# Kernel tuning notes

Hardware: AMD Instinct MI355X
Metric: run time of the kernel (lower is better)

Reference implementation:

```python
import jax, jax.numpy as jnp
import numpy as np
from jax import lax

DIM = 512          # model dim
L = 32             # img_size
N = L * L          # tokens
H = 4              # heads
C = DIM // 4       # channels per Res2Net scale
D = C // H         # per-head dim = 32 (== dim_head)
B = 8
SCALE = 32 ** -0.5  # dim_head ** -0.5
EPS = 1e-5


def setup_inputs() -> dict:
    key = jax.random.key(0)
    ks = jax.random.split(key, 13)
    nrm = lambda k, s, std: jax.random.normal(k, s, jnp.float32) * std
    uni = lambda k, s: jax.random.uniform(k, s, jnp.float32, 0.5, 1.5)
    return {
        "x": nrm(ks[0], (B, N, DIM), 1.0),
        "w_in": nrm(ks[1], (DIM, DIM), DIM ** -0.5),
        "bn1_g": uni(ks[2], (DIM,)),
        "bn1_b": nrm(ks[3], (DIM,), 0.1),
        "bn1_m": nrm(ks[4], (DIM,), 0.1),
        "bn1_v": uni(ks[5], (DIM,)),
        "w_dw": nrm(ks[6], (C, 1, 3, 3), 1.0 / 3.0),
        "w_pw": nrm(ks[7], (C, C), C ** -0.5),
        "bn2_g": uni(ks[8], (C,)),
        "bn2_b": nrm(ks[9], (C,), 0.1),
        "bn2_m": nrm(ks[10], (C,), 0.1),
        "bn2_v": uni(ks[11], (C,)),
        "w_out": nrm(ks[12], (DIM, DIM), DIM ** -0.5),
    }


def _bn(x, g, b, m, v):
    # eval-mode BatchNorm2d over NCHW
    inv = g / jnp.sqrt(v + EPS)
    return x * inv[None, :, None, None] + (b - m * inv)[None, :, None, None]


def _forward(x, w_in, bn1_g, bn1_b, bn1_m, bn1_v,
             w_dw, w_pw, bn2_g, bn2_b, bn2_m, bn2_v, w_out):
    b = x.shape[0]
    # 'b (l w) n -> b n l w'
    xi = x.transpose(0, 2, 1).reshape(b, DIM, L, L)
    # Res2Net: inconv (1x1 conv + BN)
    ident = jnp.einsum('oc,bchw->bohw', w_in, xi)
    ident = _bn(ident, bn1_g, bn1_b, bn1_m, bn1_v)
    xs = jnp.split(ident, 4, axis=1)

    def x3conv(t):
        t = lax.conv_general_dilated(
            t, w_dw, window_strides=(1, 1), padding='SAME',
            feature_group_count=C,
            dimension_numbers=('NCHW', 'OIHW', 'NCHW'))
        t = jnp.einsum('oc,bchw->bohw', w_pw, t)
        return _bn(t, bn2_g, bn2_b, bn2_m, bn2_v)

    ys = [xs[0]]
    ys.append(x3conv(xs[1]))
    ys.append(x3conv(xs[2] + ys[1]))
    ys.append(x3conv(xs[3] + ys[2]))
    y = jnp.stack(ys, axis=1)  # [b, 4, C, L, L]

    # 'b (h d) l w -> b h (l w) d' per scale; batch the 4 scales together
    qkv = y.reshape(b, 4, H, D, N).transpose(0, 1, 2, 4, 3)  # [b,4,h,n,d]
    att = jnp.einsum('bshid,bshjd->bshij', qkv, qkv) * SCALE   # [b,4,h,n,n]
    att = jax.nn.softmax(att, axis=-1)
    o = jnp.einsum('bshij,bshjd->bshid', att, qkv)             # [b,4,h,n,d]
    # cat over scales of 'b h n d -> b n (h d)' => [b, n, (s h d)] = [b, n, DIM]
    o = o.transpose(0, 3, 1, 2, 4).reshape(b, N, DIM)
    return o @ w_out.T  # Linear(dim, dim, bias=False); dropout is identity (eval)


def reference(x, w_in, bn1_g, bn1_b, bn1_m, bn1_v,
              w_dw, w_pw, bn2_g, bn2_b, bn2_m, bn2_v, w_out):
    return _forward(x, w_in, bn1_g, bn1_b, bn1_m, bn1_v,
                    w_dw, w_pw, bn2_g, bn2_b, bn2_m, bn2_v, w_out)
```

## Files before the change

### kernel.cpp

```cpp
#include <hip/hip_runtime.h>
#include <hip/hip_bf16.h>


#define DIMM 512
#define NTOK 1024
#define CC   128
#define DD   32
#define BB   8
#define EPSB 1e-5f
#define SCALE_ATT 0.17677669529663687f
#define K2EXP (SCALE_ATT * 1.4426950408889634f)
#define TJ 128

typedef __attribute__((ext_vector_type(8))) short short8;
typedef __attribute__((ext_vector_type(4))) float f32x4;

__device__ __forceinline__ unsigned short f2bf(float f) {
    unsigned int x = __float_as_uint(f);
    unsigned int r = x + 0x7fffu + ((x >> 16) & 1u);
    return (unsigned short)(r >> 16);
}
__device__ __forceinline__ unsigned int f2bf2(float lo, float hi) {
    return (unsigned int)f2bf(lo) | ((unsigned int)f2bf(hi) << 16);
}

__global__ __launch_bounds__(256) void k_mm_in(
    const float* __restrict__ w_in,
    const float* __restrict__ x,
    const float* __restrict__ g1, const float* __restrict__ b1,
    const float* __restrict__ m1, const float* __restrict__ v1,
    float* __restrict__ Y)
{
    __shared__ __align__(16) unsigned short As[128][72];
    __shared__ __align__(16) unsigned short Bs[128][72];
    const int r0 = blockIdx.x * 128;
    const int o0 = blockIdx.y * 128;
    const int b  = r0 >> 10, nloc0 = r0 & 1023;
    const int t = threadIdx.x, wid = t >> 6, lane = t & 63;
    const int l16 = lane & 15, quad = lane >> 4;
    const int wm = (wid >> 1) * 64, wn = (wid & 1) * 64;

    f32x4 acc[4][4];
#pragma unroll
    for (int i = 0; i < 4; i++)
#pragma unroll
        for (int j = 0; j < 4; j++) acc[i][j] = (f32x4){0.f, 0.f, 0.f, 0.f};

    for (int k0 = 0; k0 < DIMM; k0 += 64) {
        __syncthreads();
#pragma unroll
        for (int it = 0; it < 8; it++) {
            int flat = it * 256 + t;
            int row = flat >> 4, c4 = flat & 15;
            float4 w4 = *(const float4*)&w_in[(size_t)(o0 + row) * DIMM + k0 + c4 * 4];
            *(uint2*)&As[row][c4 * 4] = make_uint2(f2bf2(w4.x, w4.y), f2bf2(w4.z, w4.w));
            float4 x4 = *(const float4*)&x[(size_t)(r0 + row) * DIMM + k0 + c4 * 4];
            *(uint2*)&Bs[row][c4 * 4] = make_uint2(f2bf2(x4.x, x4.y), f2bf2(x4.z, x4.w));
        }
        __syncthreads();
#pragma unroll
        for (int kk = 0; kk < 2; kk++) {
            short8 af[4], bf_[4];
#pragma unroll
            for (int i = 0; i < 4; i++) af[i]  = *(const short8*)&As[wm + i * 16 + l16][kk * 32 + quad * 8];
#pragma unroll
            for (int j = 0; j < 4; j++) bf_[j] = *(const short8*)&Bs[wn + j * 16 + l16][kk * 32 + quad * 8];
#pragma unroll
            for (int i = 0; i < 4; i++)
#pragma unroll
                for (int j = 0; j < 4; j++)
                    acc[i][j] = __builtin_amdgcn_mfma_f32_16x16x32_bf16(af[i], bf_[j], acc[i][j], 0, 0, 0);
        }
    }
#pragma unroll
    for (int i = 0; i < 4; i++)
#pragma unroll
        for (int r = 0; r < 4; r++) {
            int o = o0 + wm + i * 16 + quad * 4 + r;
            float inv  = g1[o] / sqrtf(v1[o] + EPSB);
            float beta = b1[o] - m1[o] * inv;
#pragma unroll
            for (int j = 0; j < 4; j++) {
                int n = nloc0 + wn + j * 16 + l16;
                Y[((size_t)b * DIMM + o) * NTOK + n] = acc[i][j][r] * inv + beta;
            }
        }
}

__global__ __launch_bounds__(256) void k_dwconv(
    const float* __restrict__ Y, const float* __restrict__ w_dw,
    float* __restrict__ tmp, int s)
{
    __shared__ float img[34][34];
    const int c = blockIdx.x;
    const int b = blockIdx.y;
    const int t = threadIdx.x;
    for (int i = t; i < 34 * 34; i += 256) (&img[0][0])[i] = 0.f;
    __syncthreads();
    const float* src0 = Y + ((size_t)b * DIMM + s * CC + c) * NTOK;
    const float* src1 = (s >= 2) ? (Y + ((size_t)b * DIMM + (s - 1) * CC + c) * NTOK) : nullptr;
    for (int p = t; p < NTOK; p += 256) {
        float v = src0[p];
        if (src1) v += src1[p];
        img[(p >> 5) + 1][(p & 31) + 1] = v;
    }
    __syncthreads();
    float w[9];
#pragma unroll
    for (int i = 0; i < 9; i++) w[i] = w_dw[c * 9 + i];
    for (int p = t; p < NTOK; p += 256) {
        int yy = p >> 5, xx = p & 31;
        float s0 = 0.f;
#pragma unroll
        for (int ky = 0; ky < 3; ky++)
#pragma unroll
            for (int kx = 0; kx < 3; kx++)
                s0 += img[yy + ky][xx + kx] * w[ky * 3 + kx];
        tmp[((size_t)b * CC + c) * NTOK + p] = s0;
    }
}

__global__ __launch_bounds__(256) void k_mm_pw(
    const float* __restrict__ tmp, const float* __restrict__ w_pw,
    const float* __restrict__ g2, const float* __restrict__ b2,
    const float* __restrict__ m2, const float* __restrict__ v2,
    float* __restrict__ Y, int s)
{
    __shared__ __align__(16) unsigned short As[128][72];
    __shared__ __align__(16) unsigned short Bs[64][72];
    const int n0 = blockIdx.x * 64;
    const int b  = blockIdx.y;
    const int t = threadIdx.x, wid = t >> 6, lane = t & 63;
    const int l16 = lane & 15, quad = lane >> 4;
    const int wm = (wid >> 1) * 64, wn = (wid & 1) * 32;

    f32x4 acc[4][2];
#pragma unroll
    for (int i = 0; i < 4; i++) { acc[i][0] = (f32x4){0.f,0.f,0.f,0.f}; acc[i][1] = (f32x4){0.f,0.f,0.f,0.f}; }

    for (int k0 = 0; k0 < CC; k0 += 64) {
        __syncthreads();
#pragma unroll
        for (int it = 0; it < 8; it++) {
            int flat = it * 256 + t;
            int row = flat >> 4, c4 = flat & 15;
            float4 w4 = *(const float4*)&w_pw[(size_t)row * CC + k0 + c4 * 4];
            *(uint2*)&As[row][c4 * 4] = make_uint2(f2bf2(w4.x, w4.y), f2bf2(w4.z, w4.w));
        }
#pragma unroll
        for (int it = 0; it < 4; it++) {
            int flat = it * 256 + t;
            int c = flat >> 4, n4 = (flat & 15) * 4;
            float4 v = *(const float4*)&tmp[((size_t)b * CC + k0 + c) * NTOK + n0 + n4];
            Bs[n4 + 0][c] = f2bf(v.x);
            Bs[n4 + 1][c] = f2bf(v.y);
            Bs[n4 + 2][c] = f2bf(v.z);
            Bs[n4 + 3][c] = f2bf(v.w);
        }
        __syncthreads();
#pragma unroll
        for (int kk = 0; kk < 2; kk++) {
            short8 af[4], bf_[2];
#pragma unroll
            for (int i = 0; i < 4; i++) af[i]  = *(const short8*)&As[wm + i * 16 + l16][kk * 32 + quad * 8];
#pragma unroll
            for (int j = 0; j < 2; j++) bf_[j] = *(const short8*)&Bs[wn + j * 16 + l16][kk * 32 + quad * 8];
#pragma unroll
            for (int i = 0; i < 4; i++)
#pragma unroll
                for (int j = 0; j < 2; j++)
                    acc[i][j] = __builtin_amdgcn_mfma_f32_16x16x32_bf16(af[i], bf_[j], acc[i][j], 0, 0, 0);
        }
    }
#pragma unroll
    for (int i = 0; i < 4; i++)
#pragma unroll
        for (int r = 0; r < 4; r++) {
            int o = wm + i * 16 + quad * 4 + r;
            float inv  = g2[o] / sqrtf(v2[o] + EPSB);
            float beta = b2[o] - m2[o] * inv;
#pragma unroll
            for (int j = 0; j < 2; j++) {
                int n = n0 + wn + j * 16 + l16;
                Y[((size_t)b * DIMM + s * CC + o) * NTOK + n] = acc[i][j][r] * inv + beta;
            }
        }
}

__global__ __launch_bounds__(256) void k_prep(
    const float* __restrict__ Y,
    unsigned short* __restrict__ Vp,
    unsigned short* __restrict__ Qt)
{
    __shared__ float T[32][129];
    const int jt = blockIdx.x;
    const int n0 = jt * 128;
    const int g  = blockIdx.y;
    const int b = g >> 4, s = (g >> 2) & 3, h = g & 3;
    const int cb = s * CC + h * DD;
    const int t = threadIdx.x;
#pragma unroll
    for (int k = 0; k < 8; k++) {
        int idx = k * 256 + t;
        int d = idx >> 6, jp = (idx & 63) * 2;
        float2 v = *(const float2*)&Y[((size_t)b * DIMM + cb + d) * NTOK + n0 + jp];
        T[d][jp] = v.x; T[d][jp + 1] = v.y;
    }
    __syncthreads();
#pragma unroll
    for (int k = 0; k < 8; k++) {
        int idx = k * 256 + t;
        int n = idx >> 4, dp = (idx & 15) * 2;
        *(unsigned int*)&Qt[((size_t)g * NTOK + n0 + n) * DD + dp] = f2bf2(T[dp][n], T[dp + 1][n]);
    }
#pragma unroll
    for (int e2 = 0; e2 < 2; e2++) {
        int e = e2 * 256 + t;
        int sub = e >> 6, lane = e & 63;
        int quad = lane >> 4, l16 = lane & 15;
        int d  = (sub & 1) * 16 + l16;
        int jb = (sub >> 1) * 32 + quad * 4;
        uint4 v;
        v.x = f2bf2(T[d][jb + 0],  T[d][jb + 1]);
        v.y = f2bf2(T[d][jb + 2],  T[d][jb + 3]);
        v.z = f2bf2(T[d][jb + 16], T[d][jb + 17]);
        v.w = f2bf2(T[d][jb + 18], T[d][jb + 19]);
        *(uint4*)&Vp[((((size_t)g * 8 + jt) * 8 + sub) * 64 + lane) * 8] = v;
    }
}

__global__ __launch_bounds__(256) void k_attn(
    const unsigned short* __restrict__ Qtg,
    const unsigned short* __restrict__ Vp,
    unsigned short* __restrict__ Ob)
{
    const int blk = blockIdx.x;
    const int g = blk & 127, ib = blk >> 7;
    const int b = g >> 4;
    const int s = (g >> 2) & 3, h = g & 3;
    const int cb = s * CC + h * DD;
    const unsigned short* Qt = Qtg + (size_t)g * NTOK * DD;
    const unsigned short* Vg = Vp + (size_t)g * 8 * 8 * 64 * 8;
    const int t = threadIdx.x;
    const int wid = t >> 6, lane = t & 63;
    const int l16 = lane & 15, quad = lane >> 4;
    const int i = ib * 64 + wid * 16 + l16;

    const short8 qi = *(const short8*)&Qt[(size_t)i * DD + quad * 8];
    const short8 ones = {0x3F80, 0x3F80, 0x3F80, 0x3F80, 0x3F80, 0x3F80, 0x3F80, 0x3F80};

    float dq = 0.f;
#pragma unroll
    for (int e = 0; e < 8; e++) {
        float v = __uint_as_float(((unsigned int)(unsigned short)qi[e]) << 16);
        dq = fmaf(v, v, dq);
    }
    dq += __shfl_xor(dq, 16);
    dq += __shfl_xor(dq, 32);
    const float mnk = dq * K2EXP;

    f32x4 lacc = {0.f, 0.f, 0.f, 0.f};
    f32x4 oacc[2] = {{0.f,0.f,0.f,0.f},{0.f,0.f,0.f,0.f}};
    const f32x4 zero4 = {0.f, 0.f, 0.f, 0.f};

#pragma unroll 2
    for (int jt = 0; jt < 8; jt++) {
        const int j0 = jt * TJ;
        f32x4 sacc[8];
#pragma unroll
        for (int jb = 0; jb < 8; jb++) {
            short8 qj = *(const short8*)&Qt[(size_t)(j0 + jb * 16 + l16) * DD + quad * 8];
            sacc[jb] = __builtin_amdgcn_mfma_f32_16x16x32_bf16(qj, qi, zero4, 0, 0, 0);
        }

        short8 pb[4];
#pragma unroll
        for (int jb = 0; jb < 8; jb++) {
            float p0 = __builtin_amdgcn_exp2f(fmaf(sacc[jb][0], K2EXP, -mnk));
            float p1 = __builtin_amdgcn_exp2f(fmaf(sacc[jb][1], K2EXP, -mnk));
            float p2 = __builtin_amdgcn_exp2f(fmaf(sacc[jb][2], K2EXP, -mnk));
            float p3 = __builtin_amdgcn_exp2f(fmaf(sacc[jb][3], K2EXP, -mnk));
            ((unsigned int*)&pb[jb >> 1])[(jb & 1) * 2]     =
                __builtin_amdgcn_perm(__float_as_uint(p1), __float_as_uint(p0), 0x07060302u);
            ((unsigned int*)&pb[jb >> 1])[(jb & 1) * 2 + 1] =
                __builtin_amdgcn_perm(__float_as_uint(p3), __float_as_uint(p2), 0x07060302u);
        }

#pragma unroll
        for (int wp = 0; wp < 4; wp++) {
            short8 af0 = *(const short8*)&Vg[(((size_t)jt * 8 + wp * 2 + 0) * 64 + lane) * 8];
            short8 af1 = *(const short8*)&Vg[(((size_t)jt * 8 + wp * 2 + 1) * 64 + lane) * 8];
            oacc[0] = __builtin_amdgcn_mfma_f32_16x16x32_bf16(af0, pb[wp], oacc[0], 0, 0, 0);
            oacc[1] = __builtin_amdgcn_mfma_f32_16x16x32_bf16(af1, pb[wp], oacc[1], 0, 0, 0);
            lacc    = __builtin_amdgcn_mfma_f32_16x16x32_bf16(ones, pb[wp], lacc, 0, 0, 0);
        }
    }

    float invl = 1.f / lacc[0];
#pragma unroll
    for (int dblk = 0; dblk < 2; dblk++) {
        uint2 pkd;
        pkd.x = f2bf2(oacc[dblk][0] * invl, oacc[dblk][1] * invl);
        pkd.y = f2bf2(oacc[dblk][2] * invl, oacc[dblk][3] * invl);
        *(uint2*)&Ob[((size_t)b * NTOK + i) * DIMM + cb + dblk * 16 + quad * 4] = pkd;
    }
}

__global__ __launch_bounds__(256) void k_mm_out(
    const unsigned short* __restrict__ Oin,
    const float* __restrict__ w_out,
    float* __restrict__ out)
{
    __shared__ __align__(16) unsigned short As[128][72];
    __shared__ __align__(16) unsigned short Bs[128][72];
    const int r0 = blockIdx.x * 128;
    const int o0 = blockIdx.y * 128;
    const int t = threadIdx.x, wid = t >> 6, lane = t & 63;
    const int l16 = lane & 15, quad = lane >> 4;
    const int wm = (wid >> 1) * 64, wn = (wid & 1) * 64;

    f32x4 acc[4][4];
#pragma unroll
    for (int i = 0; i < 4; i++)
#pragma unroll
        for (int j = 0; j < 4; j++) acc[i][j] = (f32x4){0.f, 0.f, 0.f, 0.f};

    for (int k0 = 0; k0 < DIMM; k0 += 64) {
        __syncthreads();
#pragma unroll
        for (int q = 0; q < 4; q++) {
            int flat = q * 256 + t;
            int row = flat >> 3, c8 = flat & 7;
            *(short8*)&As[row][c8 * 8] = *(const short8*)&Oin[(size_t)(r0 + row) * DIMM + k0 + c8 * 8];
        }
#pragma unroll
        for (int it = 0; it < 8; it++) {
            int flat = it * 256 + t;
            int row = flat >> 4, c4 = flat & 15;
            float4 w4 = *(const float4*)&w_out[(size_t)(o0 + row) * DIMM + k0 + c4 * 4];
            *(uint2*)&Bs[row][c4 * 4] = make_uint2(f2bf2(w4.x, w4.y), f2bf2(w4.z, w4.w));
        }
        __syncthreads();
#pragma unroll
        for (int kk = 0; kk < 2; kk++) {
            short8 af[4], bf_[4];
#pragma unroll
            for (int i = 0; i < 4; i++) af[i]  = *(const short8*)&As[wm + i * 16 + l16][kk * 32 + quad * 8];
#pragma unroll
            for (int j = 0; j < 4; j++) bf_[j] = *(const short8*)&Bs[wn + j * 16 + l16][kk * 32 + quad * 8];
#pragma unroll
            for (int i = 0; i < 4; i++)
#pragma unroll
                for (int j = 0; j < 4; j++)
                    acc[i][j] = __builtin_amdgcn_mfma_f32_16x16x32_bf16(af[i], bf_[j], acc[i][j], 0, 0, 0);
        }
    }
#pragma unroll
    for (int i = 0; i < 4; i++)
#pragma unroll
        for (int r = 0; r < 4; r++) {
            int rr = r0 + wm + i * 16 + quad * 4 + r;
#pragma unroll
            for (int j = 0; j < 4; j++) {
                int o = o0 + wn + j * 16 + l16;
                out[(size_t)rr * DIMM + o] = acc[i][j][r];
            }
        }
}

extern "C" void kernel_launch(void* const* d_in, const int* in_sizes, int n_in,
                              void* d_out, int out_size, void* d_ws, size_t ws_size,
                              hipStream_t stream)
{
    const float* x    = (const float*)d_in[0];
    const float* w_in = (const float*)d_in[1];
    const float* g1   = (const float*)d_in[2];
    const float* b1   = (const float*)d_in[3];
    const float* m1   = (const float*)d_in[4];
    const float* v1   = (const float*)d_in[5];
    const float* wdw  = (const float*)d_in[6];
    const float* wpw  = (const float*)d_in[7];
    const float* g2   = (const float*)d_in[8];
    const float* b2   = (const float*)d_in[9];
    const float* m2   = (const float*)d_in[10];
    const float* v2   = (const float*)d_in[11];
    const float* wout = (const float*)d_in[12];
    float* out = (float*)d_out;

    char* base = (char*)d_ws;
    float*          Y   = (float*)base;
    unsigned short* Ob  = (unsigned short*)base;
    float*          tmp = (float*)(base + (size_t)16 * 1024 * 1024);
    unsigned short* Vp  = (unsigned short*)(base + (size_t)16 * 1024 * 1024);
    unsigned short* Qt  = (unsigned short*)(base + (size_t)24 * 1024 * 1024);

    k_mm_in<<<dim3(64, 4), 256, 0, stream>>>(w_in, x, g1, b1, m1, v1, Y);
    for (int s = 1; s <= 3; s++) {
        k_dwconv<<<dim3(CC, BB), 256, 0, stream>>>(Y, wdw, tmp, s);
        k_mm_pw<<<dim3(16, 8), 256, 0, stream>>>(tmp, wpw, g2, b2, m2, v2, Y, s);
    }
    k_prep<<<dim3(8, 128), 256, 0, stream>>>(Y, Vp, Qt);
    k_attn<<<dim3(2048), 256, 0, stream>>>(Qt, Vp, Ob);
    k_mm_out<<<dim3(64, 4), 256, 0, stream>>>(Ob, wout, out);
}
```

Measured before the change: 226.4 us.

## Process two query tiles per wave in attention to reuse K/V loads

Each wave in the attention kernel now handles two 16-row query tiles instead of one. Every K fragment and V fragment it loads feeds both tiles, halving the global/L2 traffic per query, and the grid shrinks from 2048 to 1024 blocks. The exp/pack step is now interleaved right after each score MFMA rather than done in a separate loop. The cost is higher register use from doubled accumulators and P fragments, which could lower occupancy.

```diff
diff --git a/kernel.cpp b/kernel.cpp
--- a/kernel.cpp
+++ b/kernel.cpp
@@ -244,65 +244,82 @@
     const int t = threadIdx.x;
     const int wid = t >> 6, lane = t & 63;
     const int l16 = lane & 15, quad = lane >> 4;
-    const int i = ib * 64 + wid * 16 + l16;
-
-    const short8 qi = *(const short8*)&Qt[(size_t)i * DD + quad * 8];
+    const int i0 = ib * 128 + wid * 16 + l16;
+    const int i1 = i0 + 64;
+
+    const short8 qi0 = *(const short8*)&Qt[(size_t)i0 * DD + quad * 8];
+    const short8 qi1 = *(const short8*)&Qt[(size_t)i1 * DD + quad * 8];
     const short8 ones = {0x3F80, 0x3F80, 0x3F80, 0x3F80, 0x3F80, 0x3F80, 0x3F80, 0x3F80};
 
-    float dq = 0.f;
+    float dq0 = 0.f, dq1 = 0.f;
 #pragma unroll
     for (int e = 0; e < 8; e++) {
-        float v = __uint_as_float(((unsigned int)(unsigned short)qi[e]) << 16);
-        dq = fmaf(v, v, dq);
-    }
-    dq += __shfl_xor(dq, 16);
-    dq += __shfl_xor(dq, 32);
-    const float mnk = dq * K2EXP;
-
-    f32x4 lacc = {0.f, 0.f, 0.f, 0.f};
-    f32x4 oacc[2] = {{0.f,0.f,0.f,0.f},{0.f,0.f,0.f,0.f}};
+        float v0 = __uint_as_float(((unsigned int)(unsigned short)qi0[e]) << 16);
+        float v1 = __uint_as_float(((unsigned int)(unsigned short)qi1[e]) << 16);
+        dq0 = fmaf(v0, v0, dq0);
+        dq1 = fmaf(v1, v1, dq1);
+    }
+    dq0 += __shfl_xor(dq0, 16); dq0 += __shfl_xor(dq0, 32);
+    dq1 += __shfl_xor(dq1, 16); dq1 += __shfl_xor(dq1, 32);
+    const float mnk0 = dq0 * K2EXP;
+    const float mnk1 = dq1 * K2EXP;
+
+    f32x4 lacc0 = {0.f,0.f,0.f,0.f}, lacc1 = {0.f,0.f,0.f,0.f};
+    f32x4 oacc0[2] = {{0.f,0.f,0.f,0.f},{0.f,0.f,0.f,0.f}};
+    f32x4 oacc1[2] = {{0.f,0.f,0.f,0.f},{0.f,0.f,0.f,0.f}};
     const f32x4 zero4 = {0.f, 0.f, 0.f, 0.f};
 
 #pragma unroll 2
     for (int jt = 0; jt < 8; jt++) {
         const int j0 = jt * TJ;
-        f32x4 sacc[8];
+        short8 pb0[4], pb1[4];
 #pragma unroll
         for (int jb = 0; jb < 8; jb++) {
             short8 qj = *(const short8*)&Qt[(size_t)(j0 + jb * 16 + l16) * DD + quad * 8];
-            sacc[jb] = __builtin_amdgcn_mfma_f32_16x16x32_bf16(qj, qi, zero4, 0, 0, 0);
-        }
-
-        short8 pb[4];
-#pragma unroll
-        for (int jb = 0; jb < 8; jb++) {
-            float p0 = __builtin_amdgcn_exp2f(fmaf(sacc[jb][0], K2EXP, -mnk));
-            float p1 = __builtin_amdgcn_exp2f(fmaf(sacc[jb][1], K2EXP, -mnk));
-            float p2 = __builtin_amdgcn_exp2f(fmaf(sacc[jb][2], K2EXP, -mnk));
-            float p3 = __builtin_amdgcn_exp2f(fmaf(sacc[jb][3], K2EXP, -mnk));
-            ((unsigned int*)&pb[jb >> 1])[(jb & 1) * 2]     =
-                __builtin_amdgcn_perm(__float_as_uint(p1), __float_as_uint(p0), 0x07060302u);
-            ((unsigned int*)&pb[jb >> 1])[(jb & 1) * 2 + 1] =
-                __builtin_amdgcn_perm(__float_as_uint(p3), __float_as_uint(p2), 0x07060302u);
+            f32x4 s0 = __builtin_amdgcn_mfma_f32_16x16x32_bf16(qj, qi0, zero4, 0, 0, 0);
+            f32x4 s1 = __builtin_amdgcn_mfma_f32_16x16x32_bf16(qj, qi1, zero4, 0, 0, 0);
+            float a0 = __builtin_amdgcn_exp2f(fmaf(s0[0], K2EXP, -mnk0));
+            float a1 = __builtin_amdgcn_exp2f(fmaf(s0[1], K2EXP, -mnk0));
+            float a2 = __builtin_amdgcn_exp2f(fmaf(s0[2], K2EXP, -mnk0));
+            float a3 = __builtin_amdgcn_exp2f(fmaf(s0[3], K2EXP, -mnk0));
+            ((unsigned int*)&pb0[jb >> 1])[(jb & 1) * 2] =
+                __builtin_amdgcn_perm(__float_as_uint(a1), __float_as_uint(a0), 0x07060302u);
+            ((unsigned int*)&pb0[jb >> 1])[(jb & 1) * 2 + 1] =
+                __builtin_amdgcn_perm(__float_as_uint(a3), __float_as_uint(a2), 0x07060302u);
+            float c0 = __builtin_amdgcn_exp2f(fmaf(s1[0], K2EXP, -mnk1));
+            float c1 = __builtin_amdgcn_exp2f(fmaf(s1[1], K2EXP, -mnk1));
+            float c2 = __builtin_amdgcn_exp2f(fmaf(s1[2], K2EXP, -mnk1));
+            float c3 = __builtin_amdgcn_exp2f(fmaf(s1[3], K2EXP, -mnk1));
+            ((unsigned int*)&pb1[jb >> 1])[(jb & 1) * 2] =
+                __builtin_amdgcn_perm(__float_as_uint(c1), __float_as_uint(c0), 0x07060302u);
+            ((unsigned int*)&pb1[jb >> 1])[(jb & 1) * 2 + 1] =
+                __builtin_amdgcn_perm(__float_as_uint(c3), __float_as_uint(c2), 0x07060302u);
         }
 
 #pragma unroll
         for (int wp = 0; wp < 4; wp++) {
             short8 af0 = *(const short8*)&Vg[(((size_t)jt * 8 + wp * 2 + 0) * 64 + lane) * 8];
             short8 af1 = *(const short8*)&Vg[(((size_t)jt * 8 + wp * 2 + 1) * 64 + lane) * 8];
-            oacc[0] = __builtin_amdgcn_mfma_f32_16x16x32_bf16(af0, pb[wp], oacc[0], 0, 0, 0);
-            oacc[1] = __builtin_amdgcn_mfma_f32_16x16x32_bf16(af1, pb[wp], oacc[1], 0, 0, 0);
-            lacc    = __builtin_amdgcn_mfma_f32_16x16x32_bf16(ones, pb[wp], lacc, 0, 0, 0);
-        }
-    }
-
-    float invl = 1.f / lacc[0];
+            oacc0[0] = __builtin_amdgcn_mfma_f32_16x16x32_bf16(af0, pb0[wp], oacc0[0], 0, 0, 0);
+            oacc0[1] = __builtin_amdgcn_mfma_f32_16x16x32_bf16(af1, pb0[wp], oacc0[1], 0, 0, 0);
+            lacc0    = __builtin_amdgcn_mfma_f32_16x16x32_bf16(ones, pb0[wp], lacc0, 0, 0, 0);
+            oacc1[0] = __builtin_amdgcn_mfma_f32_16x16x32_bf16(af0, pb1[wp], oacc1[0], 0, 0, 0);
+            oacc1[1] = __builtin_amdgcn_mfma_f32_16x16x32_bf16(af1, pb1[wp], oacc1[1], 0, 0, 0);
+            lacc1    = __builtin_amdgcn_mfma_f32_16x16x32_bf16(ones, pb1[wp], lacc1, 0, 0, 0);
+        }
+    }
+
+    float invl0 = 1.f / lacc0[0];
+    float invl1 = 1.f / lacc1[0];
 #pragma unroll
     for (int dblk = 0; dblk < 2; dblk++) {
         uint2 pkd;
-        pkd.x = f2bf2(oacc[dblk][0] * invl, oacc[dblk][1] * invl);
-        pkd.y = f2bf2(oacc[dblk][2] * invl, oacc[dblk][3] * invl);
-        *(uint2*)&Ob[((size_t)b * NTOK + i) * DIMM + cb + dblk * 16 + quad * 4] = pkd;
+        pkd.x = f2bf2(oacc0[dblk][0] * invl0, oacc0[dblk][1] * invl0);
+        pkd.y = f2bf2(oacc0[dblk][2] * invl0, oacc0[dblk][3] * invl0);
+        *(uint2*)&Ob[((size_t)b * NTOK + i0) * DIMM + cb + dblk * 16 + quad * 4] = pkd;
+        pkd.x = f2bf2(oacc1[dblk][0] * invl1, oacc1[dblk][1] * invl1);
+        pkd.y = f2bf2(oacc1[dblk][2] * invl1, oacc1[dblk][3] * invl1);
+        *(uint2*)&Ob[((size_t)b * NTOK + i1) * DIMM + cb + dblk * 16 + quad * 4] = pkd;
     }
 }
 
@@ -400,6 +417,6 @@
         k_mm_pw<<<dim3(16, 8), 256, 0, stream>>>(tmp, wpw, g2, b2, m2, v2, Y, s);
     }
     k_prep<<<dim3(8, 128), 256, 0, stream>>>(Y, Vp, Qt);
-    k_attn<<<dim3(2048), 256, 0, stream>>>(Qt, Vp, Ob);
+    k_attn<<<dim3(1024), 256, 0, stream>>>(Qt, Vp, Ob);
     k_mm_out<<<dim3(64, 4), 256, 0, stream>>>(Ob, wout, out);
 }
```

New measurement: 197.1 us. 1.15x faster.

## Process four query tiles per wave in attention to reuse K/V loads

Applied to the files above, without the earlier changes.

Each wave in the attention kernel now handles four 16-row query tiles instead of one, so every key fragment and V fragment loaded from global memory feeds four sets of MFMAs. The grid shrinks from 2048 to 512 blocks to match. The goal is to cut redundant global/L2 traffic and add independent MFMA work for latency hiding. The cost is more accumulator and P registers per lane and fewer waves in flight, which lowers occupancy.

```diff
diff --git a/kernel.cpp b/kernel.cpp
--- a/kernel.cpp
+++ b/kernel.cpp
@@ -244,65 +244,82 @@
     const int t = threadIdx.x;
     const int wid = t >> 6, lane = t & 63;
     const int l16 = lane & 15, quad = lane >> 4;
-    const int i = ib * 64 + wid * 16 + l16;
-
-    const short8 qi = *(const short8*)&Qt[(size_t)i * DD + quad * 8];
+    const int ibase = ib * 256 + wid * 16 + l16;
+
+    short8 qi[4];
+#pragma unroll
+    for (int c = 0; c < 4; c++)
+        qi[c] = *(const short8*)&Qt[(size_t)(ibase + c * 64) * DD + quad * 8];
     const short8 ones = {0x3F80, 0x3F80, 0x3F80, 0x3F80, 0x3F80, 0x3F80, 0x3F80, 0x3F80};
 
-    float dq = 0.f;
-#pragma unroll
-    for (int e = 0; e < 8; e++) {
-        float v = __uint_as_float(((unsigned int)(unsigned short)qi[e]) << 16);
-        dq = fmaf(v, v, dq);
-    }
-    dq += __shfl_xor(dq, 16);
-    dq += __shfl_xor(dq, 32);
-    const float mnk = dq * K2EXP;
-
-    f32x4 lacc = {0.f, 0.f, 0.f, 0.f};
-    f32x4 oacc[2] = {{0.f,0.f,0.f,0.f},{0.f,0.f,0.f,0.f}};
+    float mnk[4];
+#pragma unroll
+    for (int c = 0; c < 4; c++) {
+        float dq = 0.f;
+#pragma unroll
+        for (int e = 0; e < 8; e++) {
+            float v = __uint_as_float(((unsigned int)(unsigned short)qi[c][e]) << 16);
+            dq = fmaf(v, v, dq);
+        }
+        dq += __shfl_xor(dq, 16);
+        dq += __shfl_xor(dq, 32);
+        mnk[c] = dq * K2EXP;
+    }
+
+    f32x4 lacc[4];
+    f32x4 oacc[4][2];
+#pragma unroll
+    for (int c = 0; c < 4; c++) {
+        lacc[c] = (f32x4){0.f,0.f,0.f,0.f};
+        oacc[c][0] = (f32x4){0.f,0.f,0.f,0.f};
+        oacc[c][1] = (f32x4){0.f,0.f,0.f,0.f};
+    }
     const f32x4 zero4 = {0.f, 0.f, 0.f, 0.f};
 
-#pragma unroll 2
     for (int jt = 0; jt < 8; jt++) {
         const int j0 = jt * TJ;
-        f32x4 sacc[8];
+        short8 pb[4][4];
 #pragma unroll
         for (int jb = 0; jb < 8; jb++) {
             short8 qj = *(const short8*)&Qt[(size_t)(j0 + jb * 16 + l16) * DD + quad * 8];
-            sacc[jb] = __builtin_amdgcn_mfma_f32_16x16x32_bf16(qj, qi, zero4, 0, 0, 0);
-        }
-
-        short8 pb[4];
-#pragma unroll
-        for (int jb = 0; jb < 8; jb++) {
-            float p0 = __builtin_amdgcn_exp2f(fmaf(sacc[jb][0], K2EXP, -mnk));
-            float p1 = __builtin_amdgcn_exp2f(fmaf(sacc[jb][1], K2EXP, -mnk));
-            float p2 = __builtin_amdgcn_exp2f(fmaf(sacc[jb][2], K2EXP, -mnk));
-            float p3 = __builtin_amdgcn_exp2f(fmaf(sacc[jb][3], K2EXP, -mnk));
-            ((unsigned int*)&pb[jb >> 1])[(jb & 1) * 2]     =
-                __builtin_amdgcn_perm(__float_as_uint(p1), __float_as_uint(p0), 0x07060302u);
-            ((unsigned int*)&pb[jb >> 1])[(jb & 1) * 2 + 1] =
-                __builtin_amdgcn_perm(__float_as_uint(p3), __float_as_uint(p2), 0x07060302u);
+#pragma unroll
+            for (int c = 0; c < 4; c++) {
+                f32x4 sc = __builtin_amdgcn_mfma_f32_16x16x32_bf16(qj, qi[c], zero4, 0, 0, 0);
+                float p0 = __builtin_amdgcn_exp2f(fmaf(sc[0], K2EXP, -mnk[c]));
+                float p1 = __builtin_amdgcn_exp2f(fmaf(sc[1], K2EXP, -mnk[c]));
+                float p2 = __builtin_amdgcn_exp2f(fmaf(sc[2], K2EXP, -mnk[c]));
+                float p3 = __builtin_amdgcn_exp2f(fmaf(sc[3], K2EXP, -mnk[c]));
+                ((unsigned int*)&pb[c][jb >> 1])[(jb & 1) * 2] =
+                    __builtin_amdgcn_perm(__float_as_uint(p1), __float_as_uint(p0), 0x07060302u);
+                ((unsigned int*)&pb[c][jb >> 1])[(jb & 1) * 2 + 1] =
+                    __builtin_amdgcn_perm(__float_as_uint(p3), __float_as_uint(p2), 0x07060302u);
+            }
         }
 
 #pragma unroll
         for (int wp = 0; wp < 4; wp++) {
             short8 af0 = *(const short8*)&Vg[(((size_t)jt * 8 + wp * 2 + 0) * 64 + lane) * 8];
             short8 af1 = *(const short8*)&Vg[(((size_t)jt * 8 + wp * 2 + 1) * 64 + lane) * 8];
-            oacc[0] = __builtin_amdgcn_mfma_f32_16x16x32_bf16(af0, pb[wp], oacc[0], 0, 0, 0);
-            oacc[1] = __builtin_amdgcn_mfma_f32_16x16x32_bf16(af1, pb[wp], oacc[1], 0, 0, 0);
-            lacc    = __builtin_amdgcn_mfma_f32_16x16x32_bf16(ones, pb[wp], lacc, 0, 0, 0);
-        }
-    }
-
-    float invl = 1.f / lacc[0];
-#pragma unroll
-    for (int dblk = 0; dblk < 2; dblk++) {
-        uint2 pkd;
-        pkd.x = f2bf2(oacc[dblk][0] * invl, oacc[dblk][1] * invl);
-        pkd.y = f2bf2(oacc[dblk][2] * invl, oacc[dblk][3] * invl);
-        *(uint2*)&Ob[((size_t)b * NTOK + i) * DIMM + cb + dblk * 16 + quad * 4] = pkd;
+#pragma unroll
+            for (int c = 0; c < 4; c++) {
+                oacc[c][0] = __builtin_amdgcn_mfma_f32_16x16x32_bf16(af0, pb[c][wp], oacc[c][0], 0, 0, 0);
+                oacc[c][1] = __builtin_amdgcn_mfma_f32_16x16x32_bf16(af1, pb[c][wp], oacc[c][1], 0, 0, 0);
+                lacc[c]    = __builtin_amdgcn_mfma_f32_16x16x32_bf16(ones, pb[c][wp], lacc[c], 0, 0, 0);
+            }
+        }
+    }
+
+#pragma unroll
+    for (int c = 0; c < 4; c++) {
+        float invl = 1.f / lacc[c][0];
+        const int i = ibase + c * 64;
+#pragma unroll
+        for (int dblk = 0; dblk < 2; dblk++) {
+            uint2 pkd;
+            pkd.x = f2bf2(oacc[c][dblk][0] * invl, oacc[c][dblk][1] * invl);
+            pkd.y = f2bf2(oacc[c][dblk][2] * invl, oacc[c][dblk][3] * invl);
+            *(uint2*)&Ob[((size_t)b * NTOK + i) * DIMM + cb + dblk * 16 + quad * 4] = pkd;
+        }
     }
 }
 
@@ -400,6 +417,6 @@
         k_mm_pw<<<dim3(16, 8), 256, 0, stream>>>(tmp, wpw, g2, b2, m2, v2, Y, s);
     }
     k_prep<<<dim3(8, 128), 256, 0, stream>>>(Y, Vp, Qt);
-    k_attn<<<dim3(2048), 256, 0, stream>>>(Qt, Vp, Ob);
+    k_attn<<<dim3(512), 256, 0, stream>>>(Qt, Vp, Ob);
     k_mm_out<<<dim3(64, 4), 256, 0, stream>>>(Ob, wout, out);
 }
```

Result: faster. 202.2 us (-10.7%).
